# Kernel optimization log

Measured on AMD Instinct MI355X. Metric: run time of the kernel, lower is better.

The kernel has to match this reference:

```python
import math
import jax, jax.numpy as jnp
import numpy as np

B, T, C, H = 4, 2048, 1024, 16
D = C // H  # head dim = 64


def setup_inputs() -> dict:
    key = jax.random.key(0)
    ks = jax.random.split(key, 9)
    s = 1.0 / math.sqrt(C)
    return {
        "x": jax.random.normal(ks[0], (B, T, C), jnp.float32),
        "Wq": jax.random.normal(ks[1], (C, C), jnp.float32) * s,
        "bq": jax.random.normal(ks[2], (C,), jnp.float32) * 0.02,
        "Wk": jax.random.normal(ks[3], (C, C), jnp.float32) * s,
        "bk": jax.random.normal(ks[4], (C,), jnp.float32) * 0.02,
        "Wv": jax.random.normal(ks[5], (C, C), jnp.float32) * s,
        "bv": jax.random.normal(ks[6], (C,), jnp.float32) * 0.02,
        "Wo": jax.random.normal(ks[7], (C, C), jnp.float32) * s,
        "bo": jax.random.normal(ks[8], (C,), jnp.float32) * 0.02,
    }


def reference(x, Wq, bq, Wk, bk, Wv, bv, Wo, bo):
    # Projections: (B,T,C) -> (B,H,T,D)
    def heads(y):
        return y.reshape(B, T, H, D).transpose(0, 2, 1, 3)

    q = heads(x @ Wq + bq)
    k = heads(x @ Wk + bk)
    v = heads(x @ Wv + bv)

    scale = 1.0 / math.sqrt(D)
    scores = jnp.einsum("bhqd,bhkd->bhqk", q, k) * scale  # (B,H,T,T)
    causal = jnp.tril(jnp.ones((T, T), dtype=bool))
    scores = jnp.where(causal[None, None], scores, jnp.float32(-jnp.inf))
    att = jax.nn.softmax(scores, axis=-1)

    y = jnp.einsum("bhqk,bhkd->bhqd", att, v)  # (B,H,T,D)
    y = y.transpose(0, 2, 1, 3).reshape(B, T, C)
    return y @ Wo + bo
```

## Files before the change

kernel.cpp:

```cpp
#include <hip/hip_runtime.h>

#define B_ 4
#define T_ 2048
#define C_ 1024
#define H_ 16
#define D_ 64
#define M_ (B_*T_)
#define CR3 3072

typedef unsigned short u16;
typedef __attribute__((ext_vector_type(8))) short short8;
typedef __attribute__((ext_vector_type(8))) unsigned short ushort8_t;
typedef __attribute__((ext_vector_type(4))) unsigned short ushort4_t;
typedef __attribute__((ext_vector_type(4))) float floatx4;
typedef __attribute__((ext_vector_type(16))) float f32x16;
typedef __attribute__((ext_vector_type(4))) unsigned int uint4_t;

__device__ __forceinline__ u16 f2bf(float f) {
  union { float f; unsigned u; } v; v.f = f;
  unsigned r = v.u + 0x7fffu + ((v.u >> 16) & 1u);
  return (u16)(r >> 16);
}

__device__ __forceinline__ void gload16(const void* g, void* l) {
  __builtin_amdgcn_global_load_lds((__attribute__((address_space(1))) void*)(g),
                                   (__attribute__((address_space(3))) void*)(l),
                                   16, 0, 0);
}

__device__ __forceinline__ unsigned cvtpk(float lo, float hi) {
  unsigned r;
  asm("v_cvt_pk_bf16_f32 %0, %1, %2" : "=v"(r) : "v"(lo), "v"(hi));
  return r;
}

__device__ __forceinline__ void pl32swap(unsigned &a, unsigned &b) {
  asm volatile("v_permlane32_swap_b32 %0, %1" : "+v"(a), "+v"(b));
}

#define MFMA32(a, b, c) __builtin_amdgcn_mfma_f32_32x32x16_bf16(a, b, c, 0, 0, 0)
#define MFMA16(a, b, c) __builtin_amdgcn_mfma_f32_16x16x32_bf16(a, b, c, 0, 0, 0)

__global__ __launch_bounds__(256) void convx_k(const float* __restrict__ x,
                                               u16* __restrict__ o) {
  int i = (blockIdx.x * 256 + threadIdx.x) * 4;
  floatx4 v = *(const floatx4*)(x + i);
  ushort4_t r;
#pragma unroll
  for (int j = 0; j < 4; ++j) r[j] = f2bf(v[j]);
  *(ushort4_t*)(o + i) = r;
}

__global__ __launch_bounds__(256) void wconv_k(const float* __restrict__ W0,
                                               const float* __restrict__ W1,
                                               const float* __restrict__ W2,
                                               const float* __restrict__ W3,
                                               u16* __restrict__ WT) {
  __shared__ float tile[64][65];
  const float* W = blockIdx.z == 0 ? W0 : blockIdx.z == 1 ? W1 : blockIdx.z == 2 ? W2 : W3;
  const float sc = blockIdx.z == 0 ? 0.125f * 1.44269504f : 1.0f;
  u16* Wt = WT + (size_t)blockIdx.z * (C_ * C_);
  int k0 = blockIdx.x * 64, n0 = blockIdx.y * 64;
  int t = threadIdx.x;
  int r = t >> 2, c0 = (t & 3) * 16;
#pragma unroll
  for (int j = 0; j < 4; ++j) {
    floatx4 v = *(const floatx4*)(W + (size_t)(k0 + r) * C_ + n0 + c0 + j * 4);
#pragma unroll
    for (int jj = 0; jj < 4; ++jj) tile[r][c0 + j * 4 + jj] = v[jj];
  }
  __syncthreads();
  ushort8_t o0, o1;
#pragma unroll
  for (int j = 0; j < 8; ++j) o0[j] = f2bf(tile[c0 + j][r] * sc);
#pragma unroll
  for (int j = 0; j < 8; ++j) o1[j] = f2bf(tile[c0 + 8 + j][r] * sc);
  *(ushort8_t*)(Wt + (size_t)(n0 + r) * C_ + k0 + c0) = o0;
  *(ushort8_t*)(Wt + (size_t)(n0 + r) * C_ + k0 + c0 + 8) = o1;
}

__global__ __launch_bounds__(512, 2) void gemm8_k(const u16* __restrict__ A,
                                                  const u16* __restrict__ Wt,
                                                  const float* __restrict__ b0,
                                                  const float* __restrict__ b1,
                                                  const float* __restrict__ b2,
                                                  float bsc0,
                                                  u16* __restrict__ Cout) {
  __shared__ u16 lds4[49152];
  const int tid = threadIdx.x;
  const int lane = tid & 63, w = tid >> 6;
  const int wm = w >> 2, wn = w & 3;
  const int l15 = lane & 15, g = lane >> 4;

  const int bid = blockIdx.x;
  const int swz = (bid & 7) * 96 + (bid >> 3);
  const int bm = swz & 63, bn = swz >> 6;
  const int m0 = bm * 128, n0 = bn * 256;

  const int srow = tid >> 2;
  const int scol = ((tid & 3) ^ ((srow >> 1) & 3)) * 8;
  const u16* gA  = A  + (size_t)(m0 + srow) * 1024 + scol;
  const u16* gB1 = Wt + (size_t)(n0 + srow) * 1024 + scol;
  const u16* gB2 = Wt + (size_t)(n0 + 128 + srow) * 1024 + scol;

#define STAGE(KT) do { \
    u16* s_ = lds4 + ((KT) & 3) * 12288; \
    gload16(gA  + (KT) * 32, s_ + tid * 8); \
    gload16(gB1 + (KT) * 32, s_ + 4096 + tid * 8); \
    gload16(gB2 + (KT) * 32, s_ + 8192 + tid * 8); \
  } while (0)

  floatx4 acc[4][4] = {};

  STAGE(0);
  STAGE(1);

  for (int kt = 0; kt < 32; ++kt) {
    if (kt < 30) STAGE(kt + 2);
    if (kt < 30)       asm volatile("s_waitcnt vmcnt(6)" ::: "memory");
    else if (kt == 30) asm volatile("s_waitcnt vmcnt(3)" ::: "memory");
    else               asm volatile("s_waitcnt vmcnt(0)" ::: "memory");
    __builtin_amdgcn_s_barrier();

    const u16* Ab = lds4 + (kt & 3) * 12288;
    const u16* Bb = Ab + 4096;
    short8 af[4], bf[4];
#pragma unroll
    for (int mi = 0; mi < 4; ++mi) {
      int ra = wm * 64 + mi * 16 + l15;
      af[mi] = *(const short8*)(Ab + ra * 32 + ((g ^ ((ra >> 1) & 3)) << 3));
    }
#pragma unroll
    for (int ni = 0; ni < 4; ++ni) {
      int rb = wn * 64 + ni * 16 + l15;
      bf[ni] = *(const short8*)(Bb + rb * 32 + ((g ^ ((rb >> 1) & 3)) << 3));
    }
    __builtin_amdgcn_s_setprio(1);
#pragma unroll
    for (int mi = 0; mi < 4; ++mi)
#pragma unroll
      for (int ni = 0; ni < 4; ++ni)
        acc[mi][ni] = MFMA16(af[mi], bf[ni], acc[mi][ni]);
    __builtin_amdgcn_s_setprio(0);
  }

#pragma unroll
  for (int mi = 0; mi < 4; ++mi) {
    int row = m0 + wm * 64 + mi * 16 + g * 4;
#pragma unroll
    for (int ni = 0; ni < 4; ++ni) {
      int col = n0 + wn * 64 + ni * 16 + l15;
      int seg = col >> 10;
      const float* bp = seg == 0 ? b0 : seg == 1 ? b1 : b2;
      float bv = bp[col & 1023] * (seg == 0 ? bsc0 : 1.0f);
#pragma unroll
      for (int i = 0; i < 4; ++i)
        Cout[(size_t)(row + i) * CR3 + col] = f2bf(acc[mi][ni][i] + bv);
    }
  }
}

template <int OUTF32>
__global__ __launch_bounds__(256, 2) void gemm_k(const u16* __restrict__ A,
                                                 const u16* __restrict__ Wt,
                                                 const float* __restrict__ b0,
                                                 void* __restrict__ Cout, int ostride) {
  __shared__ u16 As[128 * 32];
  __shared__ u16 Bs[128 * 32];
  const int tid = threadIdx.x;
  const int w = tid >> 6, lane = tid & 63;
  const int wr = (w >> 1) * 64, wc = (w & 1) * 64;
  const int l15 = lane & 15, g = lane >> 4;
  const int m0 = blockIdx.x * 128, n0 = blockIdx.y * 128;

  floatx4 acc[4][4] = {};

  const int srow = tid >> 2;
  const int scol = ((tid & 3) ^ ((srow >> 1) & 3)) * 8;
  const u16* ga = A + (size_t)(m0 + srow) * C_ + scol;
  const u16* gb = Wt + (size_t)(n0 + srow) * C_ + scol;
  u16* lA = As + tid * 8;
  u16* lB = Bs + tid * 8;

  for (int kt = 0; kt < C_; kt += 32) {
    gload16(ga + kt, lA);
    gload16(ga + kt + (size_t)64 * C_, lA + 64 * 32);
    gload16(gb + kt, lB);
    gload16(gb + kt + (size_t)64 * C_, lB + 64 * 32);
    asm volatile("s_waitcnt vmcnt(0)" ::: "memory");
    __syncthreads();
    short8 af[4], bf[4];
#pragma unroll
    for (int i = 0; i < 4; ++i) {
      int ra = wr + i * 16 + l15;
      af[i] = *(const short8*)(As + ra * 32 + ((g ^ ((ra >> 1) & 3)) << 3));
    }
#pragma unroll
    for (int i = 0; i < 4; ++i) {
      int rb = wc + i * 16 + l15;
      bf[i] = *(const short8*)(Bs + rb * 32 + ((g ^ ((rb >> 1) & 3)) << 3));
    }
#pragma unroll
    for (int mi = 0; mi < 4; ++mi)
#pragma unroll
      for (int ni = 0; ni < 4; ++ni)
        acc[mi][ni] = MFMA16(af[mi], bf[ni], acc[mi][ni]);
    __syncthreads();
  }
#pragma unroll
  for (int mi = 0; mi < 4; ++mi) {
    int row = m0 + wr + mi * 16 + g * 4;
#pragma unroll
    for (int ni = 0; ni < 4; ++ni) {
      int col = n0 + wc + ni * 16 + l15;
      float bv = b0[col];
#pragma unroll
      for (int i = 0; i < 4; ++i) {
        float v = acc[mi][ni][i] + bv;
        if (OUTF32)
          ((float*)Cout)[(size_t)(row + i) * ostride + col] = v;
        else
          ((u16*)Cout)[(size_t)(row + i) * ostride + col] = f2bf(v);
      }
    }
  }
}

__global__ __launch_bounds__(256, 2) void attn_k(const u16* __restrict__ QKV,
                                                 u16* __restrict__ Yg) {
  __shared__ u16 Ks[2][64 * 64];
  __shared__ u16 Vt[2][64 * 64];

  const int tid = threadIdx.x;
  const int w = tid >> 6, lane = tid & 63;
  const int qi = lane & 31, h = lane >> 5;

  const int lid = blockIdx.x;
  const int a4 = lid >> 6;
  const int gq = a4 >> 2, iq = a4 & 3;
  const int jt = gq == 0 ? 15 - 2 * iq : gq == 1 ? 2 * iq : gq == 2 ? 14 - 2 * iq : 1 + 2 * iq;
  const int bh = lid & 63;
  const int nt = 2 * jt + 2;

  const size_t baseQ = (size_t)(bh >> 4) * T_ * CR3 + (size_t)(bh & 15) * D_;
  const size_t baseY = (size_t)(bh >> 4) * T_ * C_ + (size_t)(bh & 15) * D_;
  const u16* Kg = QKV + baseQ + 1024;
  const u16* Vg = QKV + baseQ + 2048;

  const int srow = tid >> 3, schunk = tid & 7;
  const int sgcol = (schunk ^ (srow & 7)) * 8;
  const u16* Kgr = Kg + (size_t)srow * CR3 + sgcol;
  const u16* Vgr = Vg + (size_t)srow * CR3 + schunk * 8;

  const int qw0 = 128 * jt + 32 * w;
  const int q_abs = qw0 + qi;

  short8 qf0, qf1, qf2, qf3;
  {
    const u16* Qr = QKV + baseQ + (size_t)q_abs * CR3 + 8 * h;
    qf0 = *(const short8*)(Qr);      qf1 = *(const short8*)(Qr + 16);
    qf2 = *(const short8*)(Qr + 32); qf3 = *(const short8*)(Qr + 48);
  }

  ushort8_t va, vbr;
  gload16(Kgr, &Ks[0][tid * 8]);
  gload16(Kgr + (size_t)32 * CR3, &Ks[0][2048 + tid * 8]);
  va = *(const ushort8_t*)(Vgr);
  vbr = *(const ushort8_t*)(Vgr + (size_t)32 * CR3);

  f32x16 y0 = {}, y1 = {};
  float l_run = 0.f;
  const float M0 = 13.0f;

  for (int t = 0; t < nt; ++t) {
    const int kv0 = t * 64;
    u16* Kb = Ks[t & 1];
    u16* Vb = Vt[t & 1];
    asm volatile("s_waitcnt vmcnt(0)" ::: "memory");
    {
      char* vbp = (char*)Vb;
#pragma unroll
      for (int j = 0; j < 8; ++j) {
        int d = schunk * 8 + j;
        int sl = ((schunk ^ j) & 7) << 4;
        *(u16*)(vbp + d * 128 + ((2 * srow) ^ sl)) = va[j];
        *(u16*)(vbp + d * 128 + ((2 * (srow + 32)) ^ sl)) = vbr[j];
      }
    }
    __syncthreads();
    if (t + 1 < nt) {
      int nkv = (t + 1) * 64;
      u16* dst = Ks[(t + 1) & 1];
      gload16(Kgr + (size_t)nkv * CR3, dst + tid * 8);
      gload16(Kgr + (size_t)(nkv + 32) * CR3, dst + 2048 + tid * 8);
      va = *(const ushort8_t*)(Vgr + (size_t)nkv * CR3);
      vbr = *(const ushort8_t*)(Vgr + (size_t)(nkv + 32) * CR3);
    }

    if (kv0 <= qw0 + 31) {
      f32x16 s0 = {}, s1 = {};
      {
        const int swq = (qi & 7) << 4;
        const char* kr0 = (const char*)Kb + qi * 128;
        const char* kr1 = (const char*)Kb + (qi + 32) * 128;
        short8 k0, k1;
        k0 = *(const short8*)(kr0 + ((16 * h) ^ swq));
        k1 = *(const short8*)(kr1 + ((16 * h) ^ swq));
        s0 = MFMA32(k0, qf0, s0); s1 = MFMA32(k1, qf0, s1);
        k0 = *(const short8*)(kr0 + ((32 + 16 * h) ^ swq));
        k1 = *(const short8*)(kr1 + ((32 + 16 * h) ^ swq));
        s0 = MFMA32(k0, qf1, s0); s1 = MFMA32(k1, qf1, s1);
        k0 = *(const short8*)(kr0 + ((64 + 16 * h) ^ swq));
        k1 = *(const short8*)(kr1 + ((64 + 16 * h) ^ swq));
        s0 = MFMA32(k0, qf2, s0); s1 = MFMA32(k1, qf2, s1);
        k0 = *(const short8*)(kr0 + ((96 + 16 * h) ^ swq));
        k1 = *(const short8*)(kr1 + ((96 + 16 * h) ^ swq));
        s0 = MFMA32(k0, qf3, s0); s1 = MFMA32(k1, qf3, s1);
      }
      if (kv0 + 63 > qw0) {
#pragma unroll
        for (int r = 0; r < 16; ++r) {
          int kvq = (r & 3) + 8 * (r >> 2) + 4 * h;
          if (kv0 + kvq > q_abs) s0[r] = -1e30f;
          if (kv0 + 32 + kvq > q_abs) s1[r] = -1e30f;
        }
      }
#pragma unroll
      for (int r = 0; r < 16; ++r) s0[r] = __builtin_amdgcn_exp2f(s0[r] - M0);
#pragma unroll
      for (int r = 0; r < 16; ++r) s1[r] = __builtin_amdgcn_exp2f(s1[r] - M0);
      {
        float a8[8];
#pragma unroll
        for (int r = 0; r < 8; ++r) a8[r] = (s0[r] + s0[r + 8]) + (s1[r] + s1[r + 8]);
#pragma unroll
        for (int r = 0; r < 4; ++r) a8[r] += a8[r + 4];
        l_run += (a8[0] + a8[1]) + (a8[2] + a8[3]);
      }
      unsigned pw[16];
      {
        unsigned a0, b0, a1, b1;
        a0 = cvtpk(s0[0], s0[1]);  b0 = cvtpk(s0[4], s0[5]);  pl32swap(a0, b0);
        a1 = cvtpk(s0[2], s0[3]);  b1 = cvtpk(s0[6], s0[7]);  pl32swap(a1, b1);
        pw[0] = a0; pw[1] = a1; pw[2] = b0; pw[3] = b1;
        a0 = cvtpk(s0[8], s0[9]);  b0 = cvtpk(s0[12], s0[13]); pl32swap(a0, b0);
        a1 = cvtpk(s0[10], s0[11]); b1 = cvtpk(s0[14], s0[15]); pl32swap(a1, b1);
        pw[4] = a0; pw[5] = a1; pw[6] = b0; pw[7] = b1;
        a0 = cvtpk(s1[0], s1[1]);  b0 = cvtpk(s1[4], s1[5]);  pl32swap(a0, b0);
        a1 = cvtpk(s1[2], s1[3]);  b1 = cvtpk(s1[6], s1[7]);  pl32swap(a1, b1);
        pw[8] = a0; pw[9] = a1; pw[10] = b0; pw[11] = b1;
        a0 = cvtpk(s1[8], s1[9]);  b0 = cvtpk(s1[12], s1[13]); pl32swap(a0, b0);
        a1 = cvtpk(s1[10], s1[11]); b1 = cvtpk(s1[14], s1[15]); pl32swap(a1, b1);
        pw[12] = a0; pw[13] = a1; pw[14] = b0; pw[15] = b1;
      }
      {
        const char* vb0 = (const char*)Vb + qi * 128;
        const char* vb1 = (const char*)Vb + (qi + 32) * 128;
        const int sx0 = (((qi >> 3) ^ qi) & 7) << 4;
        const int sx1 = sx0 ^ 0x40;
#pragma unroll
        for (int c = 0; c < 4; ++c) {
          int cb = 32 * c + 16 * h;
          uint4_t pt = {pw[c * 4 + 0], pw[c * 4 + 1], pw[c * 4 + 2], pw[c * 4 + 3]};
          short8 pa = __builtin_bit_cast(short8, pt);
          short8 v0 = *(const short8*)(vb0 + (cb ^ sx0));
          short8 v1 = *(const short8*)(vb1 + (cb ^ sx1));
          y0 = MFMA32(pa, v0, y0);
          y1 = MFMA32(pa, v1, y1);
        }
      }
    }
    __syncthreads();
  }

  l_run += __shfl_xor(l_run, 32);
  float linv = 1.0f / l_run;
#pragma unroll
  for (int r = 0; r < 16; ++r) {
    int qp = (r & 3) + 8 * (r >> 2) + 4 * h;
    float lv = __shfl(linv, qp);
    size_t row = baseY + (size_t)(qw0 + qp) * C_;
    Yg[row + qi] = f2bf(y0[r] * lv);
    Yg[row + 32 + qi] = f2bf(y1[r] * lv);
  }
}

extern "C" void kernel_launch(void* const* d_in, const int* in_sizes, int n_in,
                              void* d_out, int out_size, void* d_ws, size_t ws_size,
                              hipStream_t stream) {
  const float* x  = (const float*)d_in[0];
  const float* Wq = (const float*)d_in[1];
  const float* bq = (const float*)d_in[2];
  const float* Wk = (const float*)d_in[3];
  const float* bk = (const float*)d_in[4];
  const float* Wv = (const float*)d_in[5];
  const float* bv = (const float*)d_in[6];
  const float* Wo = (const float*)d_in[7];
  const float* bo = (const float*)d_in[8];
  float* out = (float*)d_out;

  char* ws = (char*)d_ws;
  u16* xb   = (u16*)ws;
  u16* WT   = (u16*)(ws + (size_t)16777216);
  u16* QKVb = (u16*)(ws + (size_t)25165824);
  u16* Yb = xb;

  convx_k<<<dim3(M_ * C_ / 1024), 256, 0, stream>>>(x, xb);
  wconv_k<<<dim3(16, 16, 4), 256, 0, stream>>>(Wq, Wk, Wv, Wo, WT);
  gemm8_k<<<dim3(768), 512, 0, stream>>>(xb, WT, bq, bk, bv, 0.125f * 1.44269504f, QKVb);
  attn_k<<<dim3(1024), 256, 0, stream>>>(QKVb, Yb);
  gemm_k<1><<<dim3(64, 8), 256, 0, stream>>>(Yb, WT + (size_t)3 * 1048576, bo, out, C_);
}
```

Baseline: 165.3 us.

## Pre-transpose V, triple-buffer attention K/V loads, shrink QKV GEMM to three stages

```diff
diff --git a/kernel.cpp b/kernel.cpp
--- a/kernel.cpp
+++ b/kernel.cpp
@@ -86,7 +86,7 @@
                                                   const float* __restrict__ b2,
                                                   float bsc0,
                                                   u16* __restrict__ Cout) {
-  __shared__ u16 lds4[49152];
+  __shared__ u16 lds3[36864];
   const int tid = threadIdx.x;
   const int lane = tid & 63, w = tid >> 6;
   const int wm = w >> 2, wn = w & 3;
@@ -104,7 +104,7 @@
   const u16* gB2 = Wt + (size_t)(n0 + 128 + srow) * 1024 + scol;
 
 #define STAGE(KT) do { \
-    u16* s_ = lds4 + ((KT) & 3) * 12288; \
+    u16* s_ = lds3 + ((KT) % 3) * 12288; \
     gload16(gA  + (KT) * 32, s_ + tid * 8); \
     gload16(gB1 + (KT) * 32, s_ + 4096 + tid * 8); \
     gload16(gB2 + (KT) * 32, s_ + 8192 + tid * 8); \
@@ -116,13 +116,13 @@
   STAGE(1);
 
   for (int kt = 0; kt < 32; ++kt) {
+    if (kt < 31) asm volatile("s_waitcnt vmcnt(3)" ::: "memory");
+    else         asm volatile("s_waitcnt vmcnt(0)" ::: "memory");
+    __builtin_amdgcn_s_barrier();
+    __builtin_amdgcn_sched_barrier(0);
     if (kt < 30) STAGE(kt + 2);
-    if (kt < 30)       asm volatile("s_waitcnt vmcnt(6)" ::: "memory");
-    else if (kt == 30) asm volatile("s_waitcnt vmcnt(3)" ::: "memory");
-    else               asm volatile("s_waitcnt vmcnt(0)" ::: "memory");
-    __builtin_amdgcn_s_barrier();
-
-    const u16* Ab = lds4 + (kt & 3) * 12288;
+
+    const u16* Ab = lds3 + (kt % 3) * 12288;
     const u16* Bb = Ab + 4096;
     short8 af[4], bf[4];
 #pragma unroll
@@ -160,8 +160,29 @@
   }
 }
 
+__global__ __launch_bounds__(256) void vt_k(const u16* __restrict__ QKV,
+                                            u16* __restrict__ Vtg) {
+  __shared__ unsigned tl[64][65];
+  const int tid = threadIdx.x;
+  const int bx = blockIdx.x, by = blockIdx.y;
+  const int r = tid >> 3, c8 = (tid & 7) * 8;
+  const size_t inb = ((size_t)(by >> 4) * T_ + (size_t)bx * 64) * CR3 + 2048 + (by & 15) * 64 + c8;
+  ushort8_t va = *(const ushort8_t*)(QKV + inb + (size_t)r * CR3);
+  ushort8_t vb = *(const ushort8_t*)(QKV + inb + (size_t)(r + 32) * CR3);
+#pragma unroll
+  for (int j = 0; j < 8; ++j) { tl[r][c8 + j] = va[j]; tl[r + 32][c8 + j] = vb[j]; }
+  __syncthreads();
+  ushort8_t o0, o1;
+#pragma unroll
+  for (int j = 0; j < 8; ++j) { o0[j] = (u16)tl[c8 + j][r]; o1[j] = (u16)tl[c8 + j][r + 32]; }
+  const size_t ob = ((size_t)by * 64 + r) * 2048 + bx * 64 + c8;
+  *(ushort8_t*)(Vtg + ob) = o0;
+  *(ushort8_t*)(Vtg + ob + (size_t)32 * 2048) = o1;
+}
+
 template <int OUTF32>
 __global__ __launch_bounds__(256, 2) void gemm_k(const u16* __restrict__ A,
+                                                 int astride,
                                                  const u16* __restrict__ Wt,
                                                  const float* __restrict__ b0,
                                                  void* __restrict__ Cout, int ostride) {
@@ -177,14 +198,14 @@
 
   const int srow = tid >> 2;
   const int scol = ((tid & 3) ^ ((srow >> 1) & 3)) * 8;
-  const u16* ga = A + (size_t)(m0 + srow) * C_ + scol;
+  const u16* ga = A + (size_t)(m0 + srow) * astride + scol;
   const u16* gb = Wt + (size_t)(n0 + srow) * C_ + scol;
   u16* lA = As + tid * 8;
   u16* lB = Bs + tid * 8;
 
   for (int kt = 0; kt < C_; kt += 32) {
     gload16(ga + kt, lA);
-    gload16(ga + kt + (size_t)64 * C_, lA + 64 * 32);
+    gload16(ga + kt + (size_t)64 * astride, lA + 64 * 32);
     gload16(gb + kt, lB);
     gload16(gb + kt + (size_t)64 * C_, lB + 64 * 32);
     asm volatile("s_waitcnt vmcnt(0)" ::: "memory");
@@ -226,10 +247,12 @@
   }
 }
 
-__global__ __launch_bounds__(256, 2) void attn_k(const u16* __restrict__ QKV,
-                                                 u16* __restrict__ Yg) {
-  __shared__ u16 Ks[2][64 * 64];
-  __shared__ u16 Vt[2][64 * 64];
+__global__ __launch_bounds__(256, 2) void attn_k(u16* __restrict__ QKV,
+                                                 const u16* __restrict__ Vtg) {
+  __shared__ u16 Ks3[3][64 * 64];
+  __shared__ u16 Vs3[3][64 * 64];
+  u16* KsB = &Ks3[0][0];
+  u16* VsB = &Vs3[0][0];
 
   const int tid = threadIdx.x;
   const int w = tid >> 6, lane = tid & 63;
@@ -243,14 +266,12 @@
   const int nt = 2 * jt + 2;
 
   const size_t baseQ = (size_t)(bh >> 4) * T_ * CR3 + (size_t)(bh & 15) * D_;
-  const size_t baseY = (size_t)(bh >> 4) * T_ * C_ + (size_t)(bh & 15) * D_;
   const u16* Kg = QKV + baseQ + 1024;
-  const u16* Vg = QKV + baseQ + 2048;
 
   const int srow = tid >> 3, schunk = tid & 7;
   const int sgcol = (schunk ^ (srow & 7)) * 8;
   const u16* Kgr = Kg + (size_t)srow * CR3 + sgcol;
-  const u16* Vgr = Vg + (size_t)srow * CR3 + schunk * 8;
+  const u16* Vgr = Vtg + (size_t)bh * (64 * 2048) + (size_t)srow * 2048 + sgcol;
 
   const int qw0 = 128 * jt + 32 * w;
   const int q_abs = qw0 + qi;
@@ -262,42 +283,35 @@
     qf2 = *(const short8*)(Qr + 32); qf3 = *(const short8*)(Qr + 48);
   }
 
-  ushort8_t va, vbr;
-  gload16(Kgr, &Ks[0][tid * 8]);
-  gload16(Kgr + (size_t)32 * CR3, &Ks[0][2048 + tid * 8]);
-  va = *(const ushort8_t*)(Vgr);
-  vbr = *(const ushort8_t*)(Vgr + (size_t)32 * CR3);
+#define STAGEA(T, SLOT) do { \
+    u16* kd_ = KsB + (SLOT) * 4096; \
+    u16* vd_ = VsB + (SLOT) * 4096; \
+    const size_t ko_ = (size_t)(T) * 64 * CR3; \
+    gload16(Kgr + ko_, kd_ + tid * 8); \
+    gload16(Kgr + ko_ + (size_t)32 * CR3, kd_ + 2048 + tid * 8); \
+    gload16(Vgr + (T) * 64, vd_ + tid * 8); \
+    gload16(Vgr + (T) * 64 + (size_t)32 * 2048, vd_ + 2048 + tid * 8); \
+  } while (0)
+
+  STAGEA(0, 0);
+  STAGEA(1, 1);
 
   f32x16 y0 = {}, y1 = {};
   float l_run = 0.f;
   const float M0 = 13.0f;
 
   for (int t = 0; t < nt; ++t) {
+    const int slot = t % 3;
     const int kv0 = t * 64;
-    u16* Kb = Ks[t & 1];
-    u16* Vb = Vt[t & 1];
-    asm volatile("s_waitcnt vmcnt(0)" ::: "memory");
-    {
-      char* vbp = (char*)Vb;
-#pragma unroll
-      for (int j = 0; j < 8; ++j) {
-        int d = schunk * 8 + j;
-        int sl = ((schunk ^ j) & 7) << 4;
-        *(u16*)(vbp + d * 128 + ((2 * srow) ^ sl)) = va[j];
-        *(u16*)(vbp + d * 128 + ((2 * (srow + 32)) ^ sl)) = vbr[j];
-      }
-    }
-    __syncthreads();
-    if (t + 1 < nt) {
-      int nkv = (t + 1) * 64;
-      u16* dst = Ks[(t + 1) & 1];
-      gload16(Kgr + (size_t)nkv * CR3, dst + tid * 8);
-      gload16(Kgr + (size_t)(nkv + 32) * CR3, dst + 2048 + tid * 8);
-      va = *(const ushort8_t*)(Vgr + (size_t)nkv * CR3);
-      vbr = *(const ushort8_t*)(Vgr + (size_t)(nkv + 32) * CR3);
-    }
+    if (t + 1 < nt) asm volatile("s_waitcnt vmcnt(4)" ::: "memory");
+    else            asm volatile("s_waitcnt vmcnt(0)" ::: "memory");
+    __builtin_amdgcn_s_barrier();
+    __builtin_amdgcn_sched_barrier(0);
+    if (t + 2 < nt) STAGEA(t + 2, (t + 2) % 3);
 
     if (kv0 <= qw0 + 31) {
+      const u16* Kb = KsB + slot * 4096;
+      const u16* Vb = VsB + slot * 4096;
       f32x16 s0 = {}, s1 = {};
       {
         const int swq = (qi & 7) << 4;
@@ -356,32 +370,31 @@
       {
         const char* vb0 = (const char*)Vb + qi * 128;
         const char* vb1 = (const char*)Vb + (qi + 32) * 128;
-        const int sx0 = (((qi >> 3) ^ qi) & 7) << 4;
-        const int sx1 = sx0 ^ 0x40;
+        const int sx = (qi & 7) << 4;
 #pragma unroll
         for (int c = 0; c < 4; ++c) {
           int cb = 32 * c + 16 * h;
           uint4_t pt = {pw[c * 4 + 0], pw[c * 4 + 1], pw[c * 4 + 2], pw[c * 4 + 3]};
           short8 pa = __builtin_bit_cast(short8, pt);
-          short8 v0 = *(const short8*)(vb0 + (cb ^ sx0));
-          short8 v1 = *(const short8*)(vb1 + (cb ^ sx1));
+          short8 v0 = *(const short8*)(vb0 + (cb ^ sx));
+          short8 v1 = *(const short8*)(vb1 + (cb ^ sx));
           y0 = MFMA32(pa, v0, y0);
           y1 = MFMA32(pa, v1, y1);
         }
       }
     }
-    __syncthreads();
   }
 
   l_run += __shfl_xor(l_run, 32);
   float linv = 1.0f / l_run;
+  const size_t baseY = (size_t)(bh >> 4) * T_ * CR3 + 2048 + (size_t)(bh & 15) * D_;
 #pragma unroll
   for (int r = 0; r < 16; ++r) {
     int qp = (r & 3) + 8 * (r >> 2) + 4 * h;
     float lv = __shfl(linv, qp);
-    size_t row = baseY + (size_t)(qw0 + qp) * C_;
-    Yg[row + qi] = f2bf(y0[r] * lv);
-    Yg[row + 32 + qi] = f2bf(y1[r] * lv);
+    size_t row = baseY + (size_t)(qw0 + qp) * CR3;
+    QKV[row + qi] = f2bf(y0[r] * lv);
+    QKV[row + 32 + qi] = f2bf(y1[r] * lv);
   }
 }
 
@@ -403,11 +416,13 @@
   u16* xb   = (u16*)ws;
   u16* WT   = (u16*)(ws + (size_t)16777216);
   u16* QKVb = (u16*)(ws + (size_t)25165824);
-  u16* Yb = xb;
+  u16* Vtg  = xb;
 
   convx_k<<<dim3(M_ * C_ / 1024), 256, 0, stream>>>(x, xb);
   wconv_k<<<dim3(16, 16, 4), 256, 0, stream>>>(Wq, Wk, Wv, Wo, WT);
   gemm8_k<<<dim3(768), 512, 0, stream>>>(xb, WT, bq, bk, bv, 0.125f * 1.44269504f, QKVb);
-  attn_k<<<dim3(1024), 256, 0, stream>>>(QKVb, Yb);
-  gemm_k<1><<<dim3(64, 8), 256, 0, stream>>>(Yb, WT + (size_t)3 * 1048576, bo, out, C_);
-}
+  vt_k<<<dim3(32, 64), 256, 0, stream>>>(QKVb, Vtg);
+  attn_k<<<dim3(1024), 256, 0, stream>>>(QKVb, Vtg);
+  gemm_k<1><<<dim3(64, 8), 256, 0, stream>>>(QKVb + 2048, CR3, WT + (size_t)3 * 1048576,
+                                             bo, out, C_);
+}
```

Result: slower. 172.5 us (+4.4%).

## Restructure QKV GEMM to 4 waves with 128x64 per-wave tiles and 3-stage ring

Applied to the files above, without the earlier changes.

```diff
diff --git a/kernel.cpp b/kernel.cpp
--- a/kernel.cpp
+++ b/kernel.cpp
@@ -79,55 +79,56 @@
   *(ushort8_t*)(Wt + (size_t)(n0 + r) * C_ + k0 + c0 + 8) = o1;
 }
 
-__global__ __launch_bounds__(512, 2) void gemm8_k(const u16* __restrict__ A,
+__global__ __launch_bounds__(256, 2) void gemm8_k(const u16* __restrict__ A,
                                                   const u16* __restrict__ Wt,
                                                   const float* __restrict__ b0,
                                                   const float* __restrict__ b1,
                                                   const float* __restrict__ b2,
                                                   float bsc0,
                                                   u16* __restrict__ Cout) {
-  __shared__ u16 lds4[49152];
+  __shared__ u16 lds3[36864];
   const int tid = threadIdx.x;
-  const int lane = tid & 63, w = tid >> 6;
-  const int wm = w >> 2, wn = w & 3;
+  const int lane = tid & 63, wn = tid >> 6;
   const int l15 = lane & 15, g = lane >> 4;
 
   const int bid = blockIdx.x;
   const int swz = (bid & 7) * 96 + (bid >> 3);
-  const int bm = swz & 63, bn = swz >> 6;
+  const int bn = swz >> 6, bm = swz & 63;
   const int m0 = bm * 128, n0 = bn * 256;
 
   const int srow = tid >> 2;
   const int scol = ((tid & 3) ^ ((srow >> 1) & 3)) * 8;
-  const u16* gA  = A  + (size_t)(m0 + srow) * 1024 + scol;
-  const u16* gB1 = Wt + (size_t)(n0 + srow) * 1024 + scol;
-  const u16* gB2 = Wt + (size_t)(n0 + 128 + srow) * 1024 + scol;
+  const u16* gA = A  + (size_t)(m0 + srow) * 1024 + scol;
+  const u16* gB = Wt + (size_t)(n0 + srow) * 1024 + scol;
 
 #define STAGE(KT) do { \
-    u16* s_ = lds4 + ((KT) & 3) * 12288; \
-    gload16(gA  + (KT) * 32, s_ + tid * 8); \
-    gload16(gB1 + (KT) * 32, s_ + 4096 + tid * 8); \
-    gload16(gB2 + (KT) * 32, s_ + 8192 + tid * 8); \
+    u16* s_ = lds3 + ((KT) % 3) * 12288; \
+    gload16(gA + (KT) * 32,                      s_ + tid * 8); \
+    gload16(gA + (size_t)64 * 1024 + (KT) * 32,  s_ + 2048 + tid * 8); \
+    gload16(gB + (KT) * 32,                      s_ + 4096 + tid * 8); \
+    gload16(gB + (size_t)64 * 1024 + (KT) * 32,  s_ + 6144 + tid * 8); \
+    gload16(gB + (size_t)128 * 1024 + (KT) * 32, s_ + 8192 + tid * 8); \
+    gload16(gB + (size_t)192 * 1024 + (KT) * 32, s_ + 10240 + tid * 8); \
   } while (0)
 
-  floatx4 acc[4][4] = {};
+  floatx4 acc[8][4] = {};
 
   STAGE(0);
   STAGE(1);
 
   for (int kt = 0; kt < 32; ++kt) {
+    if (kt < 31) asm volatile("s_waitcnt vmcnt(6)" ::: "memory");
+    else         asm volatile("s_waitcnt vmcnt(0)" ::: "memory");
+    __builtin_amdgcn_s_barrier();
+    __builtin_amdgcn_sched_barrier(0);
     if (kt < 30) STAGE(kt + 2);
-    if (kt < 30)       asm volatile("s_waitcnt vmcnt(6)" ::: "memory");
-    else if (kt == 30) asm volatile("s_waitcnt vmcnt(3)" ::: "memory");
-    else               asm volatile("s_waitcnt vmcnt(0)" ::: "memory");
-    __builtin_amdgcn_s_barrier();
-
-    const u16* Ab = lds4 + (kt & 3) * 12288;
+
+    const u16* Ab = lds3 + (kt % 3) * 12288;
     const u16* Bb = Ab + 4096;
-    short8 af[4], bf[4];
-#pragma unroll
-    for (int mi = 0; mi < 4; ++mi) {
-      int ra = wm * 64 + mi * 16 + l15;
+    short8 af[8], bf[4];
+#pragma unroll
+    for (int mi = 0; mi < 8; ++mi) {
+      int ra = mi * 16 + l15;
       af[mi] = *(const short8*)(Ab + ra * 32 + ((g ^ ((ra >> 1) & 3)) << 3));
     }
 #pragma unroll
@@ -137,7 +138,7 @@
     }
     __builtin_amdgcn_s_setprio(1);
 #pragma unroll
-    for (int mi = 0; mi < 4; ++mi)
+    for (int mi = 0; mi < 8; ++mi)
 #pragma unroll
       for (int ni = 0; ni < 4; ++ni)
         acc[mi][ni] = MFMA16(af[mi], bf[ni], acc[mi][ni]);
@@ -145,8 +146,8 @@
   }
 
 #pragma unroll
-  for (int mi = 0; mi < 4; ++mi) {
-    int row = m0 + wm * 64 + mi * 16 + g * 4;
+  for (int mi = 0; mi < 8; ++mi) {
+    int row = m0 + mi * 16 + g * 4;
 #pragma unroll
     for (int ni = 0; ni < 4; ++ni) {
       int col = n0 + wn * 64 + ni * 16 + l15;
@@ -162,6 +163,7 @@
 
 template <int OUTF32>
 __global__ __launch_bounds__(256, 2) void gemm_k(const u16* __restrict__ A,
+                                                 int astride,
                                                  const u16* __restrict__ Wt,
                                                  const float* __restrict__ b0,
                                                  void* __restrict__ Cout, int ostride) {
@@ -177,14 +179,14 @@
 
   const int srow = tid >> 2;
   const int scol = ((tid & 3) ^ ((srow >> 1) & 3)) * 8;
-  const u16* ga = A + (size_t)(m0 + srow) * C_ + scol;
+  const u16* ga = A + (size_t)(m0 + srow) * astride + scol;
   const u16* gb = Wt + (size_t)(n0 + srow) * C_ + scol;
   u16* lA = As + tid * 8;
   u16* lB = Bs + tid * 8;
 
   for (int kt = 0; kt < C_; kt += 32) {
     gload16(ga + kt, lA);
-    gload16(ga + kt + (size_t)64 * C_, lA + 64 * 32);
+    gload16(ga + kt + (size_t)64 * astride, lA + 64 * 32);
     gload16(gb + kt, lB);
     gload16(gb + kt + (size_t)64 * C_, lB + 64 * 32);
     asm volatile("s_waitcnt vmcnt(0)" ::: "memory");
@@ -407,7 +409,7 @@
 
   convx_k<<<dim3(M_ * C_ / 1024), 256, 0, stream>>>(x, xb);
   wconv_k<<<dim3(16, 16, 4), 256, 0, stream>>>(Wq, Wk, Wv, Wo, WT);
-  gemm8_k<<<dim3(768), 512, 0, stream>>>(xb, WT, bq, bk, bv, 0.125f * 1.44269504f, QKVb);
+  gemm8_k<<<dim3(768), 256, 0, stream>>>(xb, WT, bq, bk, bv, 0.125f * 1.44269504f, QKVb);
   attn_k<<<dim3(1024), 256, 0, stream>>>(QKVb, Yb);
-  gemm_k<1><<<dim3(64, 8), 256, 0, stream>>>(Yb, WT + (size_t)3 * 1048576, bo, out, C_);
-}
+  gemm_k<1><<<dim3(64, 8), 256, 0, stream>>>(Yb, C_, WT + (size_t)3 * 1048576, bo, out, C_);
+}
```

Result: no change. 164.2 us (-0.7%).
